# Kernel optimization log

Hardware: AMD Instinct MI355X
Metric: run time of the kernel (lower is better)

Reference implementation:

```python
import jax, jax.numpy as jnp
import numpy as np

N_HEAD = 16
INPUT_DIM = 1024
D_K = 64


def setup_inputs() -> dict:
    key = jax.random.key(0)
    k1, k2, k3 = jax.random.split(key, 3)
    x = jax.random.normal(k1, (4, 2048, INPUT_DIM), dtype=jnp.float32)
    # xavier_uniform for linear weights
    def xavier(k, shape):
        fan_out, fan_in = shape
        limit = (6.0 / (fan_in + fan_out)) ** 0.5
        return jax.random.uniform(k, shape, jnp.float32, -limit, limit)
    W_qkv = xavier(k2, (3 * D_K * N_HEAD, INPUT_DIM))
    b_qkv = jnp.zeros((3 * D_K * N_HEAD,), jnp.float32)
    W_o = xavier(k3, (D_K * N_HEAD, D_K * N_HEAD))
    b_o = jnp.zeros((D_K * N_HEAD,), jnp.float32)
    return {"x": x, "W_qkv": W_qkv, "b_qkv": b_qkv, "W_o": W_o, "b_o": b_o}


def reference(x, W_qkv, b_qkv, W_o, b_o):
    B, S, _ = x.shape
    h = x @ W_qkv.T + b_qkv                      # (B, S, 3*d_k*H)
    # NOTE: original module reshapes directly (no transpose) to (B, H, S, 3*d_k)
    h = h.reshape(B, N_HEAD, S, 3 * D_K)
    q, k, v = jnp.split(h, 3, axis=-1)           # each (B, H, S, d_k)
    scores = jnp.einsum("bhqd,bhkd->bhqk", q, k) / jnp.sqrt(jnp.float32(D_K))
    attn = jax.nn.softmax(scores, axis=-1)       # (B, H, S, S)
    o = jnp.einsum("bhqk,bhkd->bhqd", attn, v)   # (B, H, S, d_k)
    o = o.transpose(0, 2, 1, 3).reshape(B, S, N_HEAD * D_K)
    return o @ W_o.T + b_o
```

## Files before the change

kernel.cpp:

```cpp
#include <hip/hip_runtime.h>
#include <stdint.h>


typedef __attribute__((ext_vector_type(8))) short short8;
typedef __attribute__((ext_vector_type(4))) short short4v;
typedef __attribute__((ext_vector_type(4))) float f32x4;
typedef __attribute__((ext_vector_type(16))) float f32x16;

#define B_SZ 4
#define S_SZ 2048
#define H_N 16
#define DK 64
#define IN_DIM 1024
#define QKV_DIM 3072
#define MODEL 1024
#define M_ROWS (B_SZ * S_SZ)

__device__ __forceinline__ short f2bf(float f) {
    union { float f; uint32_t u; } v; v.f = f;
    uint32_t r = v.u + 0x7FFFu + ((v.u >> 16) & 1u);
    return (short)(r >> 16);
}

__device__ __forceinline__ uint32_t pk2(float a, float b) {
    return (uint32_t)(uint16_t)f2bf(a) | ((uint32_t)(uint16_t)f2bf(b) << 16);
}

__device__ __forceinline__ void gld_lds16(const void* g, void* l) {
    __builtin_amdgcn_global_load_lds(
        (const __attribute__((address_space(1))) void*)g,
        (__attribute__((address_space(3))) void*)l, 16, 0, 0);
}

__global__ __launch_bounds__(256) void cvt_kernel(
    const float* __restrict__ x, const float* __restrict__ wq,
    const float* __restrict__ wo, short* __restrict__ xb,
    short* __restrict__ wqb, short* __restrict__ wob) {
    const int NX = M_ROWS * IN_DIM / 4;
    const int NQ = QKV_DIM * IN_DIM / 4;
    const int NO = MODEL * IN_DIM / 4;
    const int total = NX + NQ + NO;
    for (int i = blockIdx.x * blockDim.x + threadIdx.x; i < total;
         i += gridDim.x * blockDim.x) {
        const f32x4* src; short4v* dst; int j;
        if (i < NX)           { src = (const f32x4*)x;  dst = (short4v*)xb;  j = i; }
        else if (i < NX + NQ) { src = (const f32x4*)wq; dst = (short4v*)wqb; j = i - NX; }
        else                  { src = (const f32x4*)wo; dst = (short4v*)wob; j = i - NX - NQ; }
        f32x4 v = src[j];
        short4v o;
        o[0] = f2bf(v[0]); o[1] = f2bf(v[1]); o[2] = f2bf(v[2]); o[3] = f2bf(v[3]);
        dst[j] = o;
    }
}

template <int MODE>
__global__ __launch_bounds__(256, 2) void gemm_bt(
    const short* __restrict__ A, const short* __restrict__ Bm,
    const float* __restrict__ bias, float* __restrict__ Cout,
    short* __restrict__ Qb, short* __restrict__ Kb, short* __restrict__ Vt,
    int M, int N, int K) {
    __shared__ short As[128 * 32];
    __shared__ short Bs[128 * 32];
    const int tid = threadIdx.x;
    const int wave = tid >> 6, lane = tid & 63;
    const int row16 = lane & 15, kgrp = lane >> 4;
    const int wm = (wave >> 1) * 64, wn = (wave & 1) * 64;
    const int bm = blockIdx.y, bn = blockIdx.x;
    const short* Ab = A + (size_t)bm * 128 * K;
    const short* Bb = Bm + (size_t)bn * 128 * K;
    f32x4 acc[4][4] = {};
    const int r0 = tid >> 2;
    const int seg = (tid & 3) * 8;
    for (int k0 = 0; k0 < K; k0 += 32) {
        gld_lds16(Ab + (size_t)r0 * K + k0 + seg, &As[r0 * 32 + seg]);
        gld_lds16(Ab + (size_t)(r0 + 64) * K + k0 + seg, &As[(r0 + 64) * 32 + seg]);
        gld_lds16(Bb + (size_t)r0 * K + k0 + seg, &Bs[r0 * 32 + seg]);
        gld_lds16(Bb + (size_t)(r0 + 64) * K + k0 + seg, &Bs[(r0 + 64) * 32 + seg]);
        __syncthreads();
        short8 af[4], bfr[4];
#pragma unroll
        for (int i = 0; i < 4; ++i)
            af[i] = *(const short8*)&As[(wm + i * 16 + row16) * 32 + kgrp * 8];
#pragma unroll
        for (int j = 0; j < 4; ++j)
            bfr[j] = *(const short8*)&Bs[(wn + j * 16 + row16) * 32 + kgrp * 8];
#pragma unroll
        for (int i = 0; i < 4; ++i)
#pragma unroll
            for (int j = 0; j < 4; ++j)
                acc[i][j] = __builtin_amdgcn_mfma_f32_16x16x32_bf16(
                    af[i], bfr[j], acc[i][j], 0, 0, 0);
        __syncthreads();
    }
#pragma unroll
    for (int j = 0; j < 4; ++j) {
        int gcol = bn * 128 + wn + j * 16 + row16;
        float bv = bias[gcol];
#pragma unroll
        for (int i = 0; i < 4; ++i) {
#pragma unroll
            for (int r = 0; r < 4; ++r) {
                int grow = bm * 128 + wm + i * 16 + kgrp * 4 + r;
                float val = acc[i][j][r] + bv;
                if (MODE == 1) {
                    Cout[(size_t)grow * N + gcol] = val;
                } else {
                    int b = grow >> 11, so = grow & 2047;
                    int hh = so >> 7, a = so & 127;
                    int rr = gcol / 192, cc = gcol - rr * 192;
                    int ss = a * 16 + rr;
                    int bh = b * H_N + hh;
                    if (cc < 64) {
                        Qb[(((size_t)bh) * S_SZ + ss) * DK + cc] = f2bf(val * 0.125f);
                    } else if (cc < 128) {
                        Kb[(((size_t)bh) * S_SZ + ss) * DK + cc - 64] = f2bf(val);
                    } else {
                        Vt[((size_t)bh * DK + (cc - 128)) * S_SZ + ss] = f2bf(val);
                    }
                }
            }
        }
    }
}

__global__ __launch_bounds__(256, 3) void attn_kernel(
    const short* __restrict__ Qg, const short* __restrict__ Kg,
    const short* __restrict__ Vtg, short* __restrict__ O) {
    __shared__ short Ks[2][64 * 64];
    __shared__ short Vs[2][64 * 64];
    const int tid = threadIdx.x;
    const int wave = tid >> 6, lane = tid & 63;
    const int q = lane & 31, hi = lane >> 5;
    const int bh = blockIdx.y;
    const int b = bh >> 4, h = bh & 15;
    const short* Qp = Qg + (size_t)bh * S_SZ * DK;
    const short* Kp = Kg + (size_t)bh * S_SZ * DK;
    const short* Vp = Vtg + (size_t)bh * DK * S_SZ;
    const int q0 = blockIdx.x * 128 + wave * 32;

    short8 qf[4];
#pragma unroll
    for (int c = 0; c < 4; ++c)
        qf[c] = *(const short8*)&Qp[(size_t)(q0 + q) * DK + c * 16 + hi * 8];

    f32x16 ot0 = {}, ot1 = {};
    float m_run = -1e30f, l_run = 0.f;

    const int sr = tid >> 2;
    const int sj = tid & 3;
    short8 kreg[2], vreg[2];

#define LOADT(KV0)                                                             \
    {                                                                          \
        _Pragma("unroll") for (int it = 0; it < 2; ++it) {                     \
            int j = sj + 4 * it;                                               \
            kreg[it] = *(const short8*)&Kp[(size_t)((KV0) + sr) * DK + j * 8]; \
            vreg[it] = *(const short8*)&Vp[(size_t)sr * S_SZ + (KV0) + j * 8]; \
        }                                                                      \
    }
#define WRITET(BUF)                                                            \
    {                                                                          \
        _Pragma("unroll") for (int it = 0; it < 2; ++it) {                     \
            int j = sj + 4 * it;                                               \
            int off = sr * 64 + ((j * 8) ^ ((sr & 7) << 3));                   \
            *(short8*)&Ks[BUF][off] = kreg[it];                                \
            *(short8*)&Vs[BUF][off] = vreg[it];                                \
        }                                                                      \
    }

    LOADT(0);
    WRITET(0);

    const int NT = S_SZ / 64;
    for (int t = 0; t < NT; ++t) {
        __syncthreads();
        const int cur = t & 1;
        const bool pf = (t + 1) < NT;
        if (pf) LOADT((t + 1) * 64);

        f32x16 st0 = {}, st1 = {};
#pragma unroll
        for (int c = 0; c < 4; ++c) {
            short8 kf0 = *(const short8*)&Ks[cur][q * 64 +
                             ((c * 16 + hi * 8) ^ ((q & 7) << 3))];
            short8 kf1 = *(const short8*)&Ks[cur][(32 + q) * 64 +
                             ((c * 16 + hi * 8) ^ (((32 + q) & 7) << 3))];
            st0 = __builtin_amdgcn_mfma_f32_32x32x16_bf16(kf0, qf[c], st0, 0, 0, 0);
            st1 = __builtin_amdgcn_mfma_f32_32x32x16_bf16(kf1, qf[c], st1, 0, 0, 0);
        }

        float pm = st0[0];
#pragma unroll
        for (int r = 1; r < 16; ++r) pm = fmaxf(pm, st0[r]);
#pragma unroll
        for (int r = 0; r < 16; ++r) pm = fmaxf(pm, st1[r]);
        pm = fmaxf(pm, __shfl_xor(pm, 32));
        float mnew = fmaxf(m_run, pm);
        float corr = __expf(m_run - mnew);
        m_run = mnew;
        float ssum = 0.f;
#pragma unroll
        for (int r = 0; r < 16; ++r) { st0[r] = __expf(st0[r] - mnew); ssum += st0[r]; }
#pragma unroll
        for (int r = 0; r < 16; ++r) { st1[r] = __expf(st1[r] - mnew); ssum += st1[r]; }
        ssum += __shfl_xor(ssum, 32);
        l_run = l_run * corr + ssum;
#pragma unroll
        for (int r = 0; r < 16; ++r) { ot0[r] *= corr; ot1[r] *= corr; }

#define PVCHUNK(ST, B0, CH)                                                    \
    {                                                                          \
        uint32_t A0 = pk2(ST[(B0) + 0], ST[(B0) + 1]);                         \
        uint32_t A1 = pk2(ST[(B0) + 2], ST[(B0) + 3]);                         \
        uint32_t B0w = pk2(ST[(B0) + 4], ST[(B0) + 5]);                        \
        uint32_t B1w = pk2(ST[(B0) + 6], ST[(B0) + 7]);                        \
        uint32_t s0 = hi ? A0 : B0w, s1 = hi ? A1 : B1w;                       \
        uint32_t r0 = (uint32_t)__shfl_xor((int)s0, 32);                       \
        uint32_t r1 = (uint32_t)__shfl_xor((int)s1, 32);                       \
        union { uint32_t u[4]; short8 s8; } pbu;                               \
        pbu.u[0] = hi ? r0 : A0;                                               \
        pbu.u[1] = hi ? r1 : A1;                                               \
        pbu.u[2] = hi ? B0w : r0;                                              \
        pbu.u[3] = hi ? B1w : r1;                                              \
        short8 vf0 = *(const short8*)&Vs[cur][q * 64 +                         \
                         (((CH) * 16 + hi * 8) ^ ((q & 7) << 3))];             \
        short8 vf1 = *(const short8*)&Vs[cur][(32 + q) * 64 +                  \
                         (((CH) * 16 + hi * 8) ^ (((32 + q) & 7) << 3))];      \
        ot0 = __builtin_amdgcn_mfma_f32_32x32x16_bf16(vf0, pbu.s8, ot0, 0, 0, 0); \
        ot1 = __builtin_amdgcn_mfma_f32_32x32x16_bf16(vf1, pbu.s8, ot1, 0, 0, 0); \
    }
        PVCHUNK(st0, 0, 0);
        PVCHUNK(st0, 8, 1);
        PVCHUNK(st1, 0, 2);
        PVCHUNK(st1, 8, 3);
#undef PVCHUNK

        if (pf) WRITET(cur ^ 1);
    }

    float inv = 1.f / l_run;
    size_t rowbase = ((size_t)b * S_SZ + (q0 + q)) * MODEL + h * DK;
#pragma unroll
    for (int i = 0; i < 4; ++i) {
        short4v v0, v1;
#pragma unroll
        for (int jj = 0; jj < 4; ++jj) {
            v0[jj] = f2bf(ot0[4 * i + jj] * inv);
            v1[jj] = f2bf(ot1[4 * i + jj] * inv);
        }
        *(short4v*)&O[rowbase + 8 * i + 4 * hi] = v0;
        *(short4v*)&O[rowbase + 32 + 8 * i + 4 * hi] = v1;
    }
#undef LOADT
#undef WRITET
}

extern "C" void kernel_launch(void* const* d_in, const int* in_sizes, int n_in,
                              void* d_out, int out_size, void* d_ws, size_t ws_size,
                              hipStream_t stream) {
    const float* x    = (const float*)d_in[0];
    const float* Wqkv = (const float*)d_in[1];
    const float* bqkv = (const float*)d_in[2];
    const float* Wo   = (const float*)d_in[3];
    const float* bo   = (const float*)d_in[4];
    float* out = (float*)d_out;
    char* ws = (char*)d_ws;

    short* xb  = (short*)(ws + 0);
    short* wqb = (short*)(ws + 16777216);
    short* wob = (short*)(ws + 23068672);
    short* Qb  = (short*)(ws + 25165824);
    short* Kb  = (short*)(ws + 41943040);
    short* Vt  = (short*)(ws + 58720256);
    short* Ob  = (short*)(ws + 0);

    cvt_kernel<<<dim3(2048), dim3(256), 0, stream>>>(x, Wqkv, Wo, xb, wqb, wob);
    gemm_bt<0><<<dim3(QKV_DIM / 128, M_ROWS / 128), dim3(256), 0, stream>>>(
        xb, wqb, bqkv, nullptr, Qb, Kb, Vt, M_ROWS, QKV_DIM, IN_DIM);
    attn_kernel<<<dim3(S_SZ / 128, B_SZ * H_N), dim3(256), 0, stream>>>(Qb, Kb, Vt, Ob);
    gemm_bt<1><<<dim3(MODEL / 128, M_ROWS / 128), dim3(256), 0, stream>>>(
        Ob, wob, bo, out, nullptr, nullptr, nullptr, M_ROWS, MODEL, IN_DIM);
}
```

Before: 273.6 us.

## Rework attention: direct global loads, exp2 softmax, lazy rescale, XCD-aware block mapping

The attention kernel drops its LDS double-buffering and has each wave load its K and V fragments straight from global memory, relying on cache reuse across the block's waves. Softmax moves to exp2, with log2e folded into the Q scale, and only rescales the running max when it grows by more than 8. The P repack uses cheaper bf16 packing and permlane32_swap, and MFMA sections get raised priority. Both GEMM and attention grids are remapped so neighbouring tiles land on the same XCD, with occupancy raised to 4 blocks per CU. The exchange is possible extra global traffic in place of LDS, and slightly different bf16 rounding.

```diff
diff --git a/kernel.cpp b/kernel.cpp
--- a/kernel.cpp
+++ b/kernel.cpp
@@ -16,14 +16,23 @@
 #define MODEL 1024
 #define M_ROWS (B_SZ * S_SZ)
 
+#define QSCALE 0.1803368801f
+
+#if __has_builtin(__builtin_amdgcn_exp2f)
+#define EXP2(x) __builtin_amdgcn_exp2f(x)
+#else
+#define EXP2(x) exp2f(x)
+#endif
+
 __device__ __forceinline__ short f2bf(float f) {
     union { float f; uint32_t u; } v; v.f = f;
     uint32_t r = v.u + 0x7FFFu + ((v.u >> 16) & 1u);
     return (short)(r >> 16);
 }
 
-__device__ __forceinline__ uint32_t pk2(float a, float b) {
-    return (uint32_t)(uint16_t)f2bf(a) | ((uint32_t)(uint16_t)f2bf(b) << 16);
+__device__ __forceinline__ uint32_t pk2f(float a, float b) {
+    union { float f; uint32_t u; } va, vb; va.f = a; vb.f = b;
+    return __builtin_amdgcn_perm(vb.u + 0x8000u, va.u + 0x8000u, 0x07060302u);
 }
 
 __device__ __forceinline__ void gld_lds16(const void* g, void* l) {
@@ -65,7 +74,10 @@
     const int wave = tid >> 6, lane = tid & 63;
     const int row16 = lane & 15, kgrp = lane >> 4;
     const int wm = (wave >> 1) * 64, wn = (wave & 1) * 64;
-    const int bm = blockIdx.y, bn = blockIdx.x;
+    const int nwg = gridDim.x * gridDim.y;
+    const int id = blockIdx.y * gridDim.x + blockIdx.x;
+    const int nid = (id & 7) * (nwg >> 3) + (id >> 3);
+    const int bn = nid % gridDim.x, bm = nid / gridDim.x;
     const short* Ab = A + (size_t)bm * 128 * K;
     const short* Bb = Bm + (size_t)bn * 128 * K;
     f32x4 acc[4][4] = {};
@@ -111,7 +123,7 @@
                     int ss = a * 16 + rr;
                     int bh = b * H_N + hh;
                     if (cc < 64) {
-                        Qb[(((size_t)bh) * S_SZ + ss) * DK + cc] = f2bf(val * 0.125f);
+                        Qb[(((size_t)bh) * S_SZ + ss) * DK + cc] = f2bf(val * QSCALE);
                     } else if (cc < 128) {
                         Kb[(((size_t)bh) * S_SZ + ss) * DK + cc - 64] = f2bf(val);
                     } else {
@@ -123,20 +135,20 @@
     }
 }
 
-__global__ __launch_bounds__(256, 3) void attn_kernel(
+__global__ __launch_bounds__(256, 4) void attn_kernel(
     const short* __restrict__ Qg, const short* __restrict__ Kg,
     const short* __restrict__ Vtg, short* __restrict__ O) {
-    __shared__ short Ks[2][64 * 64];
-    __shared__ short Vs[2][64 * 64];
     const int tid = threadIdx.x;
     const int wave = tid >> 6, lane = tid & 63;
     const int q = lane & 31, hi = lane >> 5;
-    const int bh = blockIdx.y;
+    const int id = blockIdx.x;
+    const int bh = (id & 7) * 8 + ((id >> 3) & 7);
+    const int qt = id >> 6;
     const int b = bh >> 4, h = bh & 15;
     const short* Qp = Qg + (size_t)bh * S_SZ * DK;
     const short* Kp = Kg + (size_t)bh * S_SZ * DK;
     const short* Vp = Vtg + (size_t)bh * DK * S_SZ;
-    const int q0 = blockIdx.x * 128 + wave * 32;
+    const int q0 = qt * 128 + wave * 32;
 
     short8 qf[4];
 #pragma unroll
@@ -146,96 +158,111 @@
     f32x16 ot0 = {}, ot1 = {};
     float m_run = -1e30f, l_run = 0.f;
 
-    const int sr = tid >> 2;
-    const int sj = tid & 3;
-    short8 kreg[2], vreg[2];
-
-#define LOADT(KV0)                                                             \
-    {                                                                          \
-        _Pragma("unroll") for (int it = 0; it < 2; ++it) {                     \
-            int j = sj + 4 * it;                                               \
-            kreg[it] = *(const short8*)&Kp[(size_t)((KV0) + sr) * DK + j * 8]; \
-            vreg[it] = *(const short8*)&Vp[(size_t)sr * S_SZ + (KV0) + j * 8]; \
-        }                                                                      \
-    }
-#define WRITET(BUF)                                                            \
-    {                                                                          \
-        _Pragma("unroll") for (int it = 0; it < 2; ++it) {                     \
-            int j = sj + 4 * it;                                               \
-            int off = sr * 64 + ((j * 8) ^ ((sr & 7) << 3));                   \
-            *(short8*)&Ks[BUF][off] = kreg[it];                                \
-            *(short8*)&Vs[BUF][off] = vreg[it];                                \
-        }                                                                      \
-    }
-
-    LOADT(0);
-    WRITET(0);
-
-    const int NT = S_SZ / 64;
-    for (int t = 0; t < NT; ++t) {
-        __syncthreads();
-        const int cur = t & 1;
-        const bool pf = (t + 1) < NT;
-        if (pf) LOADT((t + 1) * 64);
-
+    const short* Krow0 = Kp + (size_t)q * DK + hi * 8;
+    const short* Vrow0 = Vp + (size_t)q * S_SZ + hi * 8;
+    const short* Vrow1 = Vp + (size_t)(32 + q) * S_SZ + hi * 8;
+
+    for (int t = 0; t < S_SZ / 64; ++t) {
+        const int kv0 = t * 64;
+        short8 kf0[4], kf1[4];
+#pragma unroll
+        for (int c = 0; c < 4; ++c) {
+            kf0[c] = *(const short8*)&Krow0[(size_t)kv0 * DK + c * 16];
+            kf1[c] = *(const short8*)&Krow0[(size_t)(kv0 + 32) * DK + c * 16];
+        }
         f32x16 st0 = {}, st1 = {};
+        __builtin_amdgcn_s_setprio(1);
 #pragma unroll
         for (int c = 0; c < 4; ++c) {
-            short8 kf0 = *(const short8*)&Ks[cur][q * 64 +
-                             ((c * 16 + hi * 8) ^ ((q & 7) << 3))];
-            short8 kf1 = *(const short8*)&Ks[cur][(32 + q) * 64 +
-                             ((c * 16 + hi * 8) ^ (((32 + q) & 7) << 3))];
-            st0 = __builtin_amdgcn_mfma_f32_32x32x16_bf16(kf0, qf[c], st0, 0, 0, 0);
-            st1 = __builtin_amdgcn_mfma_f32_32x32x16_bf16(kf1, qf[c], st1, 0, 0, 0);
-        }
-
-        float pm = st0[0];
-#pragma unroll
-        for (int r = 1; r < 16; ++r) pm = fmaxf(pm, st0[r]);
-#pragma unroll
-        for (int r = 0; r < 16; ++r) pm = fmaxf(pm, st1[r]);
+            st0 = __builtin_amdgcn_mfma_f32_32x32x16_bf16(kf0[c], qf[c], st0, 0, 0, 0);
+            st1 = __builtin_amdgcn_mfma_f32_32x32x16_bf16(kf1[c], qf[c], st1, 0, 0, 0);
+        }
+        __builtin_amdgcn_s_setprio(0);
+
+        short8 vf0[4], vf1[4];
+#pragma unroll
+        for (int c = 0; c < 4; ++c) {
+            vf0[c] = *(const short8*)&Vrow0[kv0 + c * 16];
+            vf1[c] = *(const short8*)&Vrow1[kv0 + c * 16];
+        }
+
+        float ma = fmaxf(st0[0], st1[0]), mb = fmaxf(st0[1], st1[1]);
+        float mc = fmaxf(st0[2], st1[2]), md = fmaxf(st0[3], st1[3]);
+#pragma unroll
+        for (int r = 4; r < 16; r += 4) {
+            ma = fmaxf(ma, fmaxf(st0[r], st1[r]));
+            mb = fmaxf(mb, fmaxf(st0[r + 1], st1[r + 1]));
+            mc = fmaxf(mc, fmaxf(st0[r + 2], st1[r + 2]));
+            md = fmaxf(md, fmaxf(st0[r + 3], st1[r + 3]));
+        }
+        float pm = fmaxf(fmaxf(ma, mb), fmaxf(mc, md));
         pm = fmaxf(pm, __shfl_xor(pm, 32));
-        float mnew = fmaxf(m_run, pm);
-        float corr = __expf(m_run - mnew);
-        m_run = mnew;
-        float ssum = 0.f;
-#pragma unroll
-        for (int r = 0; r < 16; ++r) { st0[r] = __expf(st0[r] - mnew); ssum += st0[r]; }
-#pragma unroll
-        for (int r = 0; r < 16; ++r) { st1[r] = __expf(st1[r] - mnew); ssum += st1[r]; }
+        if (__any(pm > m_run + 8.f)) {
+            float mnew = fmaxf(m_run, pm);
+            float corr = EXP2(m_run - mnew);
+            m_run = mnew;
+            l_run *= corr;
+#pragma unroll
+            for (int r = 0; r < 16; ++r) { ot0[r] *= corr; ot1[r] *= corr; }
+        }
+        float s0 = 0.f, s1 = 0.f, s2 = 0.f, s3 = 0.f;
+#pragma unroll
+        for (int r = 0; r < 16; r += 4) {
+            st0[r] = EXP2(st0[r] - m_run);     s0 += st0[r];
+            st0[r + 1] = EXP2(st0[r + 1] - m_run); s1 += st0[r + 1];
+            st0[r + 2] = EXP2(st0[r + 2] - m_run); s2 += st0[r + 2];
+            st0[r + 3] = EXP2(st0[r + 3] - m_run); s3 += st0[r + 3];
+        }
+#pragma unroll
+        for (int r = 0; r < 16; r += 4) {
+            st1[r] = EXP2(st1[r] - m_run);     s0 += st1[r];
+            st1[r + 1] = EXP2(st1[r + 1] - m_run); s1 += st1[r + 1];
+            st1[r + 2] = EXP2(st1[r + 2] - m_run); s2 += st1[r + 2];
+            st1[r + 3] = EXP2(st1[r + 3] - m_run); s3 += st1[r + 3];
+        }
+        float ssum = (s0 + s1) + (s2 + s3);
         ssum += __shfl_xor(ssum, 32);
-        l_run = l_run * corr + ssum;
-#pragma unroll
-        for (int r = 0; r < 16; ++r) { ot0[r] *= corr; ot1[r] *= corr; }
-
+        l_run += ssum;
+
+        __builtin_amdgcn_s_setprio(1);
+#if __has_builtin(__builtin_amdgcn_permlane32_swap)
 #define PVCHUNK(ST, B0, CH)                                                    \
     {                                                                          \
-        uint32_t A0 = pk2(ST[(B0) + 0], ST[(B0) + 1]);                         \
-        uint32_t A1 = pk2(ST[(B0) + 2], ST[(B0) + 3]);                         \
-        uint32_t B0w = pk2(ST[(B0) + 4], ST[(B0) + 5]);                        \
-        uint32_t B1w = pk2(ST[(B0) + 6], ST[(B0) + 7]);                        \
-        uint32_t s0 = hi ? A0 : B0w, s1 = hi ? A1 : B1w;                       \
-        uint32_t r0 = (uint32_t)__shfl_xor((int)s0, 32);                       \
-        uint32_t r1 = (uint32_t)__shfl_xor((int)s1, 32);                       \
+        uint32_t A01 = pk2f(ST[(B0) + 0], ST[(B0) + 1]);                       \
+        uint32_t A23 = pk2f(ST[(B0) + 2], ST[(B0) + 3]);                       \
+        uint32_t B45 = pk2f(ST[(B0) + 4], ST[(B0) + 5]);                       \
+        uint32_t B67 = pk2f(ST[(B0) + 6], ST[(B0) + 7]);                       \
+        auto sw0 = __builtin_amdgcn_permlane32_swap(A01, B45, false, false);   \
+        auto sw1 = __builtin_amdgcn_permlane32_swap(A23, B67, false, false);   \
         union { uint32_t u[4]; short8 s8; } pbu;                               \
-        pbu.u[0] = hi ? r0 : A0;                                               \
-        pbu.u[1] = hi ? r1 : A1;                                               \
-        pbu.u[2] = hi ? B0w : r0;                                              \
-        pbu.u[3] = hi ? B1w : r1;                                              \
-        short8 vf0 = *(const short8*)&Vs[cur][q * 64 +                         \
-                         (((CH) * 16 + hi * 8) ^ ((q & 7) << 3))];             \
-        short8 vf1 = *(const short8*)&Vs[cur][(32 + q) * 64 +                  \
-                         (((CH) * 16 + hi * 8) ^ (((32 + q) & 7) << 3))];      \
-        ot0 = __builtin_amdgcn_mfma_f32_32x32x16_bf16(vf0, pbu.s8, ot0, 0, 0, 0); \
-        ot1 = __builtin_amdgcn_mfma_f32_32x32x16_bf16(vf1, pbu.s8, ot1, 0, 0, 0); \
-    }
+        pbu.u[0] = sw0[0]; pbu.u[1] = sw1[0];                                  \
+        pbu.u[2] = sw0[1]; pbu.u[3] = sw1[1];                                  \
+        ot0 = __builtin_amdgcn_mfma_f32_32x32x16_bf16(vf0[CH], pbu.s8, ot0, 0, 0, 0); \
+        ot1 = __builtin_amdgcn_mfma_f32_32x32x16_bf16(vf1[CH], pbu.s8, ot1, 0, 0, 0); \
+    }
+#else
+#define PVCHUNK(ST, B0, CH)                                                    \
+    {                                                                          \
+        uint32_t A01 = pk2f(ST[(B0) + 0], ST[(B0) + 1]);                       \
+        uint32_t A23 = pk2f(ST[(B0) + 2], ST[(B0) + 3]);                       \
+        uint32_t B45 = pk2f(ST[(B0) + 4], ST[(B0) + 5]);                       \
+        uint32_t B67 = pk2f(ST[(B0) + 6], ST[(B0) + 7]);                       \
+        uint32_t t0 = hi ? A01 : B45, t1 = hi ? A23 : B67;                     \
+        uint32_t r0 = (uint32_t)__shfl_xor((int)t0, 32);                       \
+        uint32_t r1 = (uint32_t)__shfl_xor((int)t1, 32);                       \
+        union { uint32_t u[4]; short8 s8; } pbu;                               \
+        pbu.u[0] = hi ? r0 : A01; pbu.u[1] = hi ? r1 : A23;                    \
+        pbu.u[2] = hi ? B45 : r0; pbu.u[3] = hi ? B67 : r1;                    \
+        ot0 = __builtin_amdgcn_mfma_f32_32x32x16_bf16(vf0[CH], pbu.s8, ot0, 0, 0, 0); \
+        ot1 = __builtin_amdgcn_mfma_f32_32x32x16_bf16(vf1[CH], pbu.s8, ot1, 0, 0, 0); \
+    }
+#endif
         PVCHUNK(st0, 0, 0);
         PVCHUNK(st0, 8, 1);
         PVCHUNK(st1, 0, 2);
         PVCHUNK(st1, 8, 3);
 #undef PVCHUNK
-
-        if (pf) WRITET(cur ^ 1);
+        __builtin_amdgcn_s_setprio(0);
     }
 
     float inv = 1.f / l_run;
@@ -251,8 +278,6 @@
         *(short4v*)&O[rowbase + 8 * i + 4 * hi] = v0;
         *(short4v*)&O[rowbase + 32 + 8 * i + 4 * hi] = v1;
     }
-#undef LOADT
-#undef WRITET
 }
 
 extern "C" void kernel_launch(void* const* d_in, const int* in_sizes, int n_in,
@@ -277,7 +302,7 @@
     cvt_kernel<<<dim3(2048), dim3(256), 0, stream>>>(x, Wqkv, Wo, xb, wqb, wob);
     gemm_bt<0><<<dim3(QKV_DIM / 128, M_ROWS / 128), dim3(256), 0, stream>>>(
         xb, wqb, bqkv, nullptr, Qb, Kb, Vt, M_ROWS, QKV_DIM, IN_DIM);
-    attn_kernel<<<dim3(S_SZ / 128, B_SZ * H_N), dim3(256), 0, stream>>>(Qb, Kb, Vt, Ob);
+    attn_kernel<<<dim3(1024), dim3(256), 0, stream>>>(Qb, Kb, Vt, Ob);
     gemm_bt<1><<<dim3(MODEL / 128, M_ROWS / 128), dim3(256), 0, stream>>>(
         Ob, wob, bo, out, nullptr, nullptr, nullptr, M_ROWS, MODEL, IN_DIM);
 }
```

New measurement: 399.4 us. +46.0%, slower.
